# Performance work log

Hardware: AMD Instinct MI355X
Metric: run time of the kernel (lower is better)

## Reference

```python
import jax, jax.numpy as jnp
import numpy as np

N, D = 16384, 32            # nodes, max neighbors (0-padded)
INP, U = 256, 128           # input_units, units
R, ENT = 8, 8               # relations, entity types (relation/entity id 0 = padding for relations)


def setup_inputs() -> dict:
    key = jax.random.key(0)
    ks = jax.random.split(key, 12)
    s = 0.05  # scale learned params for numerical sanity (torch init is raw randn)
    return {
        "node_state": jax.random.normal(ks[0], (N, INP), dtype=jnp.float32),
        "adjacency": jax.random.randint(ks[1], (N, D), 0, N + 1, dtype=jnp.int32),  # 0 = pad row
        "point_enc": jax.random.randint(ks[2], (N,), 0, ENT, dtype=jnp.int32),
        "relation_enc": jax.random.randint(ks[3], (N, D), 0, R, dtype=jnp.int32),   # 0 = pad edge
        "point_enc_w": jax.random.normal(ks[4], (ENT, INP, U), dtype=jnp.float32) * s,
        "relation_enc_w": jax.random.normal(ks[5], (R, U, U), dtype=jnp.float32) * s,
        "q_w": jax.random.normal(ks[6], (U, U), dtype=jnp.float32) * s,
        "k_w": jax.random.normal(ks[7], (U, U), dtype=jnp.float32) * s,
        "v_w": jax.random.normal(ks[8], (U, U), dtype=jnp.float32) * s,
        "fc_w": jax.random.normal(ks[9], (U, U), dtype=jnp.float32) * s,
        "fc_b": jax.random.normal(ks[10], (U,), dtype=jnp.float32) * s,
    }


def reference(node_state, adjacency, point_enc, relation_enc,
              point_enc_w, relation_enc_w, q_w, k_w, v_w, fc_w, fc_b):
    ent, inp, u = point_enc_w.shape
    r_cnt = relation_enc_w.shape[0]
    dt = node_state.dtype

    # center = node_state @ point_enc_w[point_enc]; loop over small fixed entity set
    # to avoid materializing an (N, INP, U) gathered weight tensor.
    center = jnp.zeros((node_state.shape[0], u), dtype=dt)
    for e in range(ent):
        center = center + jnp.where(point_enc[:, None] == e,
                                    node_state @ point_enc_w[e], 0.0)

    # prepend zero row: adjacency index 0 == padding neighbor
    padded = jnp.concatenate([jnp.zeros((1, u), dtype=dt), center], axis=0)  # (N+1, U)
    x = padded[adjacency]  # (N, D, U) gathered neighbor embeddings

    # neighbors = x @ relation_enc_w[relation_enc]; per-relation GEMM + mask
    # (same math as the per-edge gathered matmul, without the E*U*U blowup)
    neighbors = jnp.zeros_like(x)
    for r in range(r_cnt):
        neighbors = neighbors + jnp.where(relation_enc[..., None] == r,
                                          jnp.einsum('ndu,uv->ndv', x, relation_enc_w[r]), 0.0)

    scale = u ** 0.5
    q = (center @ q_w) / scale                               # (N, U)
    k = jnp.einsum('ndu,uv->ndv', neighbors, k_w) / scale    # (N, D, U)
    v = jnp.einsum('ndu,uv->ndv', neighbors, v_w)            # (N, D, U)

    scores = jnp.einsum('nu,ndu->nd', q, k)                  # (N, D)
    scores = jnp.where(relation_enc == 0, jnp.asarray(-1e9, dt), scores)
    attn = jax.nn.softmax(scores, axis=-1)                   # over neighbors
    agg = jnp.einsum('nd,ndu->nu', attn, v)                  # (N, U)

    return center + jax.nn.relu(agg @ fc_w + fc_b)           # (N, U)
```

## Files before the change

kernel.cpp:

```cpp
#include <hip/hip_runtime.h>

#define NNODE 16384
#define DD 32
#define INPC 256
#define UC 128
#define RC 8
#define EC 8

typedef __attribute__((ext_vector_type(8))) short short8;
typedef __attribute__((ext_vector_type(4))) float float4v;
typedef __attribute__((ext_vector_type(4))) unsigned uint4v;

__device__ __forceinline__ unsigned short f2bf(float f) {
    unsigned u = __builtin_bit_cast(unsigned, f);
    unsigned r = (u + 0x7FFFu + ((u >> 16) & 1u)) >> 16;
    return (unsigned short)r;
}
__device__ __forceinline__ float bf2f(unsigned short s) { return __builtin_bit_cast(float, (unsigned)s << 16); }

__device__ __forceinline__ short8 ld8bf(const float* p) {
    float4 v0 = *(const float4*)p;
    float4 v1 = *(const float4*)(p + 4);
    short8 a;
    a[0] = (short)f2bf(v0.x); a[1] = (short)f2bf(v0.y);
    a[2] = (short)f2bf(v0.z); a[3] = (short)f2bf(v0.w);
    a[4] = (short)f2bf(v1.x); a[5] = (short)f2bf(v1.y);
    a[6] = (short)f2bf(v1.z); a[7] = (short)f2bf(v1.w);
    return a;
}

__device__ __forceinline__ int bfrag_idx(int k, int col, int nct) {
    int ks = k >> 5, ct = col >> 4;
    int l = (((k >> 3) & 3) << 4) | (col & 15);
    return (((ks * nct + ct) << 6) + l) * 8 + (k & 7);
}

__global__ void k_setup(const float* __restrict__ pew, const float* __restrict__ qw,
                        const float* __restrict__ kw, const float* __restrict__ relw,
                        const float* __restrict__ vw, const float* __restrict__ fcw,
                        const int* __restrict__ pe,
                        unsigned short* __restrict__ pewfrag,
                        unsigned short* __restrict__ BallQfrag, unsigned short* __restrict__ RVFfrag,
                        int* __restrict__ blockhist) {
    __shared__ unsigned short stage_s[128 * 132];
    __shared__ unsigned short mat_s[16 * 136];
    __shared__ int hh[8];
    int b = blockIdx.x;
    if (b < 1024) {
        int id = b * 256 + threadIdx.x;
        int e = id >> 15, k = (id >> 7) & 255, col = id & 127;
        pewfrag[(e << 15) + bfrag_idx(k, col, 8)] = f2bf(pew[id]);
        return;
    }
    if (b < 1088) {
        int pb = b - 1024;
        int r = pb & 7, i0 = (pb >> 3) * 16;
        int w = threadIdx.x >> 6, l = threadIdx.x & 63;
        int mrow = l & 15, kgrp = (l >> 4) << 3;
        const float* R = relw + r * (UC * UC);

        float4v accP[2] = {};
        #pragma unroll
        for (int ks = 0; ks < 4; ++ks) {
            short8 a = ld8bf(&qw[(i0 + mrow) * UC + ks * 32 + kgrp]);
            #pragma unroll
            for (int ci = 0; ci < 2; ++ci) {
                int ct = w * 2 + ci;
                short8 bf = ld8bf(&kw[(ct * 16 + mrow) * UC + ks * 32 + kgrp]);
                accP[ci] = __builtin_amdgcn_mfma_f32_16x16x32_bf16(a, bf, accP[ci], 0, 0, 0);
            }
        }
        #pragma unroll
        for (int ci = 0; ci < 2; ++ci)
            #pragma unroll
            for (int reg = 0; reg < 4; ++reg) {
                int row = ((l >> 4) << 2) + reg;
                int col = (w * 2 + ci) * 16 + mrow;
                mat_s[row * 136 + col] = f2bf(accP[ci][reg] * (1.0f / 128.0f));
            }
        for (int it = 0; it < 16; ++it) {
            int idx = it * 256 + threadIdx.x;
            int row = idx >> 5, col = (idx & 31) * 4;
            float4 v = *(const float4*)&vw[row * UC + col];
            uint2 o;
            o.x = (unsigned)f2bf(v.x) | ((unsigned)f2bf(v.y) << 16);
            o.y = (unsigned)f2bf(v.z) | ((unsigned)f2bf(v.w) << 16);
            *(uint2*)&stage_s[row * 132 + col] = o;
        }
        __syncthreads();

        float4v accM[2] = {}, accV[2] = {};
        #pragma unroll
        for (int ks = 0; ks < 4; ++ks) {
            short8 aM = *(const short8*)&mat_s[mrow * 136 + ks * 32 + kgrp];
            short8 aV = ld8bf(&R[(i0 + mrow) * UC + ks * 32 + kgrp]);
            #pragma unroll
            for (int ci = 0; ci < 2; ++ci) {
                int ct = w * 2 + ci;
                short8 bM = ld8bf(&R[(ct * 16 + mrow) * UC + ks * 32 + kgrp]);
                accM[ci] = __builtin_amdgcn_mfma_f32_16x16x32_bf16(aM, bM, accM[ci], 0, 0, 0);
                uint4v pv;
                #pragma unroll
                for (int jp = 0; jp < 4; ++jp) {
                    unsigned e0 = stage_s[(ks * 32 + kgrp + jp * 2) * 132 + ct * 16 + mrow];
                    unsigned e1 = stage_s[(ks * 32 + kgrp + jp * 2 + 1) * 132 + ct * 16 + mrow];
                    pv[jp] = e0 | (e1 << 16);
                }
                accV[ci] = __builtin_amdgcn_mfma_f32_16x16x32_bf16(
                    aV, __builtin_bit_cast(short8, pv), accV[ci], 0, 0, 0);
            }
        }
        #pragma unroll
        for (int ci = 0; ci < 2; ++ci)
            #pragma unroll
            for (int reg = 0; reg < 4; ++reg) {
                int i = i0 + ((l >> 4) << 2) + reg;
                int col = r * 128 + (w * 2 + ci) * 16 + mrow;
                BallQfrag[bfrag_idx(i, col, 64)] = f2bf(accM[ci][reg]);
            }
        __syncthreads();
        #pragma unroll
        for (int ci = 0; ci < 2; ++ci)
            #pragma unroll
            for (int reg = 0; reg < 4; ++reg)
                mat_s[(((l >> 4) << 2) + reg) * 136 + (w * 2 + ci) * 16 + mrow] = f2bf(accV[ci][reg]);
        for (int it = 0; it < 16; ++it) {
            int idx = it * 256 + threadIdx.x;
            int row = idx >> 5, col = (idx & 31) * 4;
            float4 v = *(const float4*)&fcw[row * UC + col];
            uint2 o;
            o.x = (unsigned)f2bf(v.x) | ((unsigned)f2bf(v.y) << 16);
            o.y = (unsigned)f2bf(v.z) | ((unsigned)f2bf(v.w) << 16);
            *(uint2*)&stage_s[row * 132 + col] = o;
        }
        __syncthreads();

        float4v accF[2] = {};
        #pragma unroll
        for (int ks = 0; ks < 4; ++ks) {
            short8 aF = *(const short8*)&mat_s[mrow * 136 + ks * 32 + kgrp];
            #pragma unroll
            for (int ci = 0; ci < 2; ++ci) {
                int ct = w * 2 + ci;
                uint4v pv;
                #pragma unroll
                for (int jp = 0; jp < 4; ++jp) {
                    unsigned e0 = stage_s[(ks * 32 + kgrp + jp * 2) * 132 + ct * 16 + mrow];
                    unsigned e1 = stage_s[(ks * 32 + kgrp + jp * 2 + 1) * 132 + ct * 16 + mrow];
                    pv[jp] = e0 | (e1 << 16);
                }
                accF[ci] = __builtin_amdgcn_mfma_f32_16x16x32_bf16(
                    aF, __builtin_bit_cast(short8, pv), accF[ci], 0, 0, 0);
            }
        }
        #pragma unroll
        for (int ci = 0; ci < 2; ++ci)
            #pragma unroll
            for (int reg = 0; reg < 4; ++reg) {
                int i = i0 + ((l >> 4) << 2) + reg;
                int col = (w * 2 + ci) * 16 + mrow;
                RVFfrag[bfrag_idx(r * 128 + i, col, 8)] = f2bf(accF[ci][reg]);
            }
        return;
    }
    {
        int hb = b - 1088;
        if (threadIdx.x < 8) hh[threadIdx.x] = 0;
        __syncthreads();
        atomicAdd(&hh[pe[hb * 256 + threadIdx.x]], 1);
        __syncthreads();
        if (threadIdx.x < 8) blockhist[hb * 8 + threadIdx.x] = hh[threadIdx.x];
    }
}

__global__ void k_scatter(const int* __restrict__ pe, const int* __restrict__ blockhist,
                          int* __restrict__ list, int* __restrict__ cnt, int* __restrict__ basep) {
    __shared__ int boff[8];
    __shared__ int totS[8], exS[8];
    __shared__ int wavecnt[4 * 8];
    int t = threadIdx.x, w = t >> 6, l = t & 63;
    if (w == 0) {
        #pragma unroll
        for (int e = 0; e < 8; ++e) {
            int h = blockhist[l * 8 + e];
            int pref = h;
            #pragma unroll
            for (int off = 1; off < 64; off <<= 1) {
                int v = __shfl_up(pref, off, 64);
                pref += (l >= off) ? v : 0;
            }
            if (l == (int)blockIdx.x) exS[e] = pref - h;
            if (l == 63) totS[e] = pref;
        }
    }
    __syncthreads();
    if (t == 0) {
        int run = 0;
        #pragma unroll
        for (int e = 0; e < 8; ++e) {
            boff[e] = run + exS[e];
            if (blockIdx.x == 0) { basep[e] = run; cnt[e] = totS[e]; }
            run += totS[e];
        }
    }
    __syncthreads();
    int n = blockIdx.x * 256 + t;
    int e = pe[n];
    unsigned long long mymask = 0;
    #pragma unroll
    for (int r = 0; r < 8; ++r) {
        unsigned long long m = __ballot(e == r);
        if (e == r) mymask = m;
        if (l == r) wavecnt[w * 8 + r] = (int)__popcll(m);
    }
    __syncthreads();
    int off = 0;
    for (int w2 = 0; w2 < w; ++w2) off += wavecnt[w2 * 8 + e];
    unsigned long long ltmask = (1ull << l) - 1ull;
    int rank = (int)__popcll(mymask & ltmask);
    list[boff[e] + off + rank] = n;
}

__global__ __launch_bounds__(256, 4)
void k_center(const float* __restrict__ ns, const unsigned short* __restrict__ pewfrag,
              const int* __restrict__ list, const int* __restrict__ cnt,
              const int* __restrict__ base, unsigned short* __restrict__ center_bf) {
    int e = blockIdx.y;
    int c = cnt[e];
    int start = blockIdx.x * 16;
    if (start >= c) return;
    int w = threadIdx.x >> 6, l = threadIdx.x & 63;

    int rid = list[base[e] + min(start + (l & 15), c - 1)];

    float4v acc[2] = {};
    const unsigned short* pf = pewfrag + ((size_t)e << 15);
    #pragma unroll
    for (int ks = 0; ks < 8; ++ks) {
        short8 a = ld8bf(&ns[(size_t)rid * 256 + ks * 32 + ((l >> 4) << 3)]);
        #pragma unroll
        for (int ci = 0; ci < 2; ++ci) {
            int ct = w * 2 + ci;
            short8 b = *(const short8*)&pf[(((ks * 8 + ct) << 6) + l) * 8];
            acc[ci] = __builtin_amdgcn_mfma_f32_16x16x32_bf16(a, b, acc[ci], 0, 0, 0);
        }
    }
    #pragma unroll
    for (int reg = 0; reg < 4; ++reg) {
        int row16 = start + ((l >> 4) << 2) + reg;
        if (row16 < c) {
            int gid = list[base[e] + row16];
            #pragma unroll
            for (int ci = 0; ci < 2; ++ci)
                center_bf[(size_t)gid * 128 + (w * 2 + ci) * 16 + (l & 15)] = f2bf(acc[ci][reg]);
        }
    }
}

#define QSTRIDE 1096
__global__ __launch_bounds__(256, 2)
void k_final(const unsigned short* __restrict__ center_bf,
             const unsigned short* __restrict__ BallQfrag,
             const unsigned short* __restrict__ RVFfrag,
             const int* __restrict__ adj, const int* __restrict__ rel,
             const float* __restrict__ fcb, float* __restrict__ out) {
    __shared__ unsigned short qlds[16 * QSTRIDE];
    __shared__ __align__(16) unsigned short xs[4][4096];
    __shared__ unsigned edata[4][32];
    int w = threadIdx.x >> 6, l = threadIdx.x & 63;
    int n0 = blockIdx.x * 16;

    int aiq[4][2], rvq[4][2], myrow[4];
    #pragma unroll
    for (int q = 0; q < 4; ++q) {
        int n = n0 + w * 4 + q;
        #pragma unroll
        for (int t = 0; t < 2; ++t) {
            aiq[q][t] = adj[n * DD + t * 16 + (l & 15)];
            rvq[q][t] = rel[n * DD + t * 16 + (l & 15)];
        }
    }
    #pragma unroll
    for (int q = 0; q < 4; ++q) {
        int r0 = aiq[q][0] > 0 ? aiq[q][0] - 1 : 0;
        int r1 = aiq[q][1] > 0 ? aiq[q][1] - 1 : 0;
        int s0 = __shfl(r0, (l >> 1) & 15, 64);
        int s1 = __shfl(r1, (l >> 1) & 15, 64);
        myrow[q] = (l >= 32) ? s1 : s0;
    }
    uint4v sb[8];
    #pragma unroll
    for (int i = 0; i < 8; ++i)
        sb[i] = *(const uint4v*)&center_bf[(size_t)myrow[0] * 128 + ((l & 1) + 2 * i) * 8];

    {
        short8 a[4];
        #pragma unroll
        for (int ks = 0; ks < 4; ++ks)
            a[ks] = *(const short8*)&center_bf[(size_t)(n0 + (l & 15)) * 128 + ks * 32 + ((l >> 4) << 3)];
        for (int ci = 0; ci < 16; ++ci) {
            int ct = w * 16 + ci;
            float4v acc = {};
            #pragma unroll
            for (int ks = 0; ks < 4; ++ks) {
                short8 b = *(const short8*)&BallQfrag[(((ks * 64 + ct) << 6) + l) * 8];
                acc = __builtin_amdgcn_mfma_f32_16x16x32_bf16(a[ks], b, acc, 0, 0, 0);
            }
            int r = ct >> 3;
            int ch = (ct & 7) * 16 + (l & 15);
            #pragma unroll
            for (int reg = 0; reg < 4; ++reg) {
                int rn = ((l >> 4) << 2) + reg;
                qlds[rn * QSTRIDE + r * 136 + ch] = f2bf(acc[reg]);
            }
        }
    }
    __syncthreads();

    #pragma unroll
    for (int q = 0; q < 4; ++q) {
        int tn = w * 4 + q;
        int ai[2] = {aiq[q][0], aiq[q][1]};
        int rv[2] = {rvq[q][0], rvq[q][1]};

        #pragma unroll
        for (int i = 0; i < 8; ++i)
            *(uint4v*)&xs[w][i * 512 + (l >> 3) * 64
                             + ((((l >> 1) & 3) ^ ((l >> 3) & 3))) * 16 + (l & 1) * 8] = sb[i];
        if (q < 3) {
            #pragma unroll
            for (int i = 0; i < 8; ++i)
                sb[i] = *(const uint4v*)&center_bf[(size_t)myrow[q + 1] * 128 + ((l & 1) + 2 * i) * 8];
        }

        float4v sc[2] = {};
        #pragma unroll
        for (int ks = 0; ks < 4; ++ks) {
            short8 qb = *(const short8*)&qlds[tn * QSTRIDE + (l & 7) * 136 + ks * 32 + ((l >> 4) << 3)];
            #pragma unroll
            for (int t = 0; t < 2; ++t) {
                short8 xa = *(const short8*)&xs[w][(2 * ks + (l >> 5)) * 512
                                  + (4 * t + ((l >> 2) & 3)) * 64
                                  + (((l & 3) ^ ((l >> 2) & 3))) * 16 + ((l >> 4) & 1) * 8];
                sc[t] = __builtin_amdgcn_mfma_f32_16x16x32_bf16(xa, qb, sc[t], 0, 0, 0);
            }
        }
        float sel[2][4];
        int ai2[2][4];
        #pragma unroll
        for (int t = 0; t < 2; ++t)
            #pragma unroll
            for (int reg = 0; reg < 4; ++reg) {
                int e2l = ((l >> 4) & 3) * 4 + reg;
                int rd2 = __shfl(rv[t], (l & 48) | e2l, 64);
                ai2[t][reg] = __shfl(ai[t], (l & 48) | e2l, 64);
                float s = __shfl(sc[t][reg], (l & 48) | rd2, 64);
                if (ai2[t][reg] == 0) s = 0.f;
                if (rd2 == 0) s = -1e9f;
                sel[t][reg] = s;
            }
        float mx = sel[0][0];
        #pragma unroll
        for (int t = 0; t < 2; ++t)
            #pragma unroll
            for (int reg = 0; reg < 4; ++reg) mx = fmaxf(mx, sel[t][reg]);
        mx = fmaxf(mx, __shfl_xor(mx, 16, 64));
        mx = fmaxf(mx, __shfl_xor(mx, 32, 64));
        float at[2][4];
        float sm = 0.f;
        #pragma unroll
        for (int t = 0; t < 2; ++t)
            #pragma unroll
            for (int reg = 0; reg < 4; ++reg) {
                at[t][reg] = __expf(sel[t][reg] - mx);
                sm += at[t][reg];
            }
        sm += __shfl_xor(sm, 16, 64);
        sm += __shfl_xor(sm, 32, 64);
        float inv = 1.0f / sm;
        #pragma unroll
        for (int t = 0; t < 2; ++t)
            #pragma unroll
            for (int reg = 0; reg < 4; ++reg) {
                at[t][reg] *= inv;
                if (ai2[t][reg] == 0) at[t][reg] = 0.f;
            }

        #pragma unroll
        for (int rg = 0; rg < 4; ++rg) {
            if (l == (l >> 4) * 20 + rg) {
                #pragma unroll
                for (int t = 0; t < 2; ++t)
                    edata[w][t * 16 + (l & 15)] = (unsigned)f2bf(at[t][rg]) | ((unsigned)rv[t] << 16);
            }
        }

        unsigned aw[4];
        #pragma unroll
        for (int jp = 0; jp < 4; ++jp) {
            unsigned m0 = edata[w][((l >> 4) << 3) + jp * 2];
            unsigned m1 = edata[w][((l >> 4) << 3) + jp * 2 + 1];
            unsigned s0 = ((m0 >> 16) == (unsigned)(l & 15)) ? (m0 & 0xFFFFu) : 0u;
            unsigned s1 = ((m1 >> 16) == (unsigned)(l & 15)) ? (m1 & 0xFFFFu) : 0u;
            aw[jp] = s0 | (s1 << 16);
        }
        uint4v av = {aw[0], aw[1], aw[2], aw[3]};
        short8 afrag = __builtin_bit_cast(short8, av);

        #pragma unroll
        for (int ct = 0; ct < 8; ++ct) {
            unsigned short p[8];
            #pragma unroll
            for (int jj = 0; jj < 8; ++jj) {
                int st = (l >> 4) * 2 + (jj >> 2);
                int slot = (jj & 3) ^ (st & 3);
                p[jj] = xs[w][ct * 512 + st * 64 + slot * 16 + (l & 15)];
            }
            uint4v bv = {(unsigned)p[0] | ((unsigned)p[1] << 16),
                         (unsigned)p[2] | ((unsigned)p[3] << 16),
                         (unsigned)p[4] | ((unsigned)p[5] << 16),
                         (unsigned)p[6] | ((unsigned)p[7] << 16)};
            float4v zc = {};
            float4v acc = __builtin_amdgcn_mfma_f32_16x16x32_bf16(
                afrag, __builtin_bit_cast(short8, bv), zc, 0, 0, 0);
            if (l < 32) {
                int rbase = (l >> 4) << 2;
                #pragma unroll
                for (int reg = 0; reg < 4; ++reg)
                    qlds[tn * QSTRIDE + (rbase + reg) * 136 + ct * 16 + (l & 15)] = f2bf(acc[reg]);
            }
        }
    }
    __syncthreads();

    #pragma unroll
    for (int ci = 0; ci < 2; ++ci) {
        int ct = w * 2 + ci;
        float4v acc = {};
        #pragma unroll 4
        for (int ks = 0; ks < 32; ++ks) {
            short8 a = *(const short8*)&qlds[(l & 15) * QSTRIDE + (ks >> 2) * 136
                                             + (ks & 3) * 32 + ((l >> 4) << 3)];
            short8 b = *(const short8*)&RVFfrag[(((ks * 8 + ct) << 6) + l) * 8];
            acc = __builtin_amdgcn_mfma_f32_16x16x32_bf16(a, b, acc, 0, 0, 0);
        }
        int col = ct * 16 + (l & 15);
        float bb = fcb[col];
        #pragma unroll
        for (int reg = 0; reg < 4; ++reg) {
            int n = n0 + ((l >> 4) << 2) + reg;
            float v = acc[reg] + bb;
            v = v > 0.f ? v : 0.f;
            out[(size_t)n * 128 + col] = bf2f(center_bf[(size_t)n * 128 + col]) + v;
        }
    }
}

extern "C" void kernel_launch(void* const* d_in, const int* in_sizes, int n_in,
                              void* d_out, int out_size, void* d_ws, size_t ws_size,
                              hipStream_t stream) {
    const float* node_state = (const float*)d_in[0];
    const int*   adjacency  = (const int*)d_in[1];
    const int*   point_enc  = (const int*)d_in[2];
    const int*   relation   = (const int*)d_in[3];
    const float* pew        = (const float*)d_in[4];
    const float* relw       = (const float*)d_in[5];
    const float* qw         = (const float*)d_in[6];
    const float* kw         = (const float*)d_in[7];
    const float* vw         = (const float*)d_in[8];
    const float* fcw        = (const float*)d_in[9];
    const float* fcb        = (const float*)d_in[10];
    float* out = (float*)d_out;

    char* ws = (char*)d_ws;
    unsigned short* BallQfrag = (unsigned short*)ws;  ws += 128 * 1024 * 2;
    unsigned short* RVFfrag   = (unsigned short*)ws;  ws += 1024 * 128 * 2;
    unsigned short* center_bf = (unsigned short*)ws;  ws += (size_t)NNODE * 128 * 2;
    unsigned short* pewfrag   = (unsigned short*)ws;  ws += 8 * 32768 * 2;
    int* blockhist            = (int*)ws;             ws += 64 * 8 * 4;
    int* cnt                  = (int*)ws;             ws += 32;
    int* basep                = (int*)ws;             ws += 32;
    int* list                 = (int*)ws;             ws += NNODE * 4;

    k_setup<<<1152, 256, 0, stream>>>(pew, qw, kw, relw, vw, fcw, point_enc,
                                      pewfrag, BallQfrag, RVFfrag, blockhist);
    k_scatter<<<64, 256, 0, stream>>>(point_enc, blockhist, list, cnt, basep);
    k_center<<<dim3(192, 8), 256, 0, stream>>>(node_state, pewfrag, list, cnt, basep, center_bf);
    k_final<<<NNODE / 16, 256, 0, stream>>>(center_bf, BallQfrag, RVFfrag,
                                            adjacency, relation, fcb, out);
}
```

Before: 160.2 us.

## Load score MFMA operands directly from global and pair-pack neighbor rows in LDS

The score MFMA now reads neighbor embedding fragments straight from global memory into registers, and prefetches the next node's fragments, instead of reading them back from an LDS staging tile. The LDS tile used for the attention-weighted aggregation is rebuilt with a new layout that interleaves pairs of neighbor rows into 32-bit words. The B-fragment for that MFMA then needs four 32-bit LDS reads instead of eight 16-bit reads plus packing. The trade-off is more global loads per node and more register pressure from the prefetched fragments.

```diff
diff --git a/kernel.cpp b/kernel.cpp
--- a/kernel.cpp
+++ b/kernel.cpp
@@ -270,7 +270,7 @@
     int w = threadIdx.x >> 6, l = threadIdx.x & 63;
     int n0 = blockIdx.x * 16;
 
-    int aiq[4][2], rvq[4][2], myrow[4];
+    int aiq[4][2], rvq[4][2], rvrow[4][2];
     #pragma unroll
     for (int q = 0; q < 4; ++q) {
         int n = n0 + w * 4 + q;
@@ -278,20 +278,16 @@
         for (int t = 0; t < 2; ++t) {
             aiq[q][t] = adj[n * DD + t * 16 + (l & 15)];
             rvq[q][t] = rel[n * DD + t * 16 + (l & 15)];
-        }
-    }
-    #pragma unroll
-    for (int q = 0; q < 4; ++q) {
-        int r0 = aiq[q][0] > 0 ? aiq[q][0] - 1 : 0;
-        int r1 = aiq[q][1] > 0 ? aiq[q][1] - 1 : 0;
-        int s0 = __shfl(r0, (l >> 1) & 15, 64);
-        int s1 = __shfl(r1, (l >> 1) & 15, 64);
-        myrow[q] = (l >= 32) ? s1 : s0;
-    }
-    uint4v sb[8];
-    #pragma unroll
-    for (int i = 0; i < 8; ++i)
-        sb[i] = *(const uint4v*)&center_bf[(size_t)myrow[0] * 128 + ((l & 1) + 2 * i) * 8];
+            rvrow[q][t] = aiq[q][t] > 0 ? aiq[q][t] - 1 : 0;
+        }
+    }
+
+    short8 xp[2][4];
+    #pragma unroll
+    for (int t = 0; t < 2; ++t)
+        #pragma unroll
+        for (int ks = 0; ks < 4; ++ks)
+            xp[t][ks] = *(const short8*)&center_bf[(size_t)rvrow[0][t] * 128 + ks * 32 + ((l >> 4) << 3)];
 
     {
         short8 a[4];
@@ -317,20 +313,25 @@
     }
     __syncthreads();
 
+    unsigned* xsw = (unsigned*)&xs[w][0];
+
     #pragma unroll
     for (int q = 0; q < 4; ++q) {
         int tn = w * 4 + q;
         int ai[2] = {aiq[q][0], aiq[q][1]};
         int rv[2] = {rvq[q][0], rvq[q][1]};
 
-        #pragma unroll
-        for (int i = 0; i < 8; ++i)
-            *(uint4v*)&xs[w][i * 512 + (l >> 3) * 64
-                             + ((((l >> 1) & 3) ^ ((l >> 3) & 3))) * 16 + (l & 1) * 8] = sb[i];
-        if (q < 3) {
-            #pragma unroll
-            for (int i = 0; i < 8; ++i)
-                sb[i] = *(const uint4v*)&center_bf[(size_t)myrow[q + 1] * 128 + ((l & 1) + 2 * i) * 8];
+        int srcA = (l >> 1) & 14, srcB = srcA | 1;
+        int a0 = __shfl(rvrow[q][0], srcA, 64), a1 = __shfl(rvrow[q][1], srcA, 64);
+        int b0 = __shfl(rvrow[q][0], srcB, 64), b1 = __shfl(rvrow[q][1], srcB, 64);
+        int rA = (l >= 32) ? a1 : a0;
+        int rB = (l >= 32) ? b1 : b0;
+        uint4v sbA[4], sbB[4];
+        #pragma unroll
+        for (int i = 0; i < 4; ++i) {
+            int c = (l & 3) + 4 * i;
+            sbA[i] = *(const uint4v*)&center_bf[(size_t)rA * 128 + c * 8];
+            sbB[i] = *(const uint4v*)&center_bf[(size_t)rB * 128 + c * 8];
         }
 
         float4v sc[2] = {};
@@ -338,13 +339,18 @@
         for (int ks = 0; ks < 4; ++ks) {
             short8 qb = *(const short8*)&qlds[tn * QSTRIDE + (l & 7) * 136 + ks * 32 + ((l >> 4) << 3)];
             #pragma unroll
-            for (int t = 0; t < 2; ++t) {
-                short8 xa = *(const short8*)&xs[w][(2 * ks + (l >> 5)) * 512
-                                  + (4 * t + ((l >> 2) & 3)) * 64
-                                  + (((l & 3) ^ ((l >> 2) & 3))) * 16 + ((l >> 4) & 1) * 8];
-                sc[t] = __builtin_amdgcn_mfma_f32_16x16x32_bf16(xa, qb, sc[t], 0, 0, 0);
-            }
-        }
+            for (int t = 0; t < 2; ++t)
+                sc[t] = __builtin_amdgcn_mfma_f32_16x16x32_bf16(xp[t][ks], qb, sc[t], 0, 0, 0);
+        }
+        if (q < 3) {
+            #pragma unroll
+            for (int t = 0; t < 2; ++t)
+                #pragma unroll
+                for (int ks = 0; ks < 4; ++ks)
+                    xp[t][ks] = *(const short8*)&center_bf[(size_t)rvrow[q + 1][t] * 128
+                                                           + ks * 32 + ((l >> 4) << 3)];
+        }
+
         float sel[2][4];
         int ai2[2][4];
         #pragma unroll
@@ -407,19 +413,36 @@
         uint4v av = {aw[0], aw[1], aw[2], aw[3]};
         short8 afrag = __builtin_bit_cast(short8, av);
 
+        {
+            unsigned p = (unsigned)(l >> 2);
+            unsigned xorb = ((l >> 4) & 1u) << 4;
+            #pragma unroll
+            for (int i = 0; i < 4; ++i) {
+                int c = (l & 3) + 4 * i;
+                unsigned o[8];
+                #pragma unroll
+                for (int k = 0; k < 4; ++k) {
+                    unsigned A = sbA[i][k], B = sbB[i][k];
+                    o[2 * k]     = (A & 0xFFFFu) | (B << 16);
+                    o[2 * k + 1] = (A >> 16) | (B & 0xFFFF0000u);
+                }
+                unsigned d = p * 128u + (((unsigned)(c * 8)) ^ xorb);
+                uint4v lo = {o[0], o[1], o[2], o[3]};
+                uint4v hi = {o[4], o[5], o[6], o[7]};
+                *(uint4v*)(xsw + d) = lo;
+                *(uint4v*)(xsw + d + 4) = hi;
+            }
+        }
+
         #pragma unroll
         for (int ct = 0; ct < 8; ++ct) {
-            unsigned short p[8];
-            #pragma unroll
-            for (int jj = 0; jj < 8; ++jj) {
-                int st = (l >> 4) * 2 + (jj >> 2);
-                int slot = (jj & 3) ^ (st & 3);
-                p[jj] = xs[w][ct * 512 + st * 64 + slot * 16 + (l & 15)];
-            }
-            uint4v bv = {(unsigned)p[0] | ((unsigned)p[1] << 16),
-                         (unsigned)p[2] | ((unsigned)p[3] << 16),
-                         (unsigned)p[4] | ((unsigned)p[5] << 16),
-                         (unsigned)p[6] | ((unsigned)p[7] << 16)};
+            uint4v bv;
+            #pragma unroll
+            for (int m = 0; m < 4; ++m) {
+                unsigned p2 = (unsigned)((l >> 4) * 4 + m);
+                unsigned ch = (unsigned)(ct * 16 + (l & 15));
+                bv[m] = xsw[p2 * 128u + (ch ^ (((l >> 4) & 1u) << 4))];
+            }
             float4v zc = {};
             float4v acc = __builtin_amdgcn_mfma_f32_16x16x32_bf16(
                 afrag, __builtin_bit_cast(short8, bv), zc, 0, 0, 0);
```

New measurement: 166.1 us. 3.7% more time.

## Load neighbor rows directly as MFMA fragments and keep softmax in registers

Applied to the files above, without the earlier changes.

Neighbor center rows are now loaded straight into MFMA operand layout (xp) and used from registers for the score MFMA, swapping operand order so each lane holds one edge's scores. The LDS copy uses a new row-major swizzle and is read only by the aggregation step. Softmax is done with lane-per-edge shuffles instead of an 8-way gather, and the edata LDS exchange is replaced by shuffles. The final FC loop is restructured to share A loads across two output tiles. In exchange it uses more registers (32 VGPRs for xp) and does strided 16-bit LDS reads that may hit bank conflicts.

```diff
diff --git a/kernel.cpp b/kernel.cpp
--- a/kernel.cpp
+++ b/kernel.cpp
@@ -266,11 +266,10 @@
              const float* __restrict__ fcb, float* __restrict__ out) {
     __shared__ unsigned short qlds[16 * QSTRIDE];
     __shared__ __align__(16) unsigned short xs[4][4096];
-    __shared__ unsigned edata[4][32];
     int w = threadIdx.x >> 6, l = threadIdx.x & 63;
     int n0 = blockIdx.x * 16;
 
-    int aiq[4][2], rvq[4][2], myrow[4];
+    int aiq[4][2], rvq[4][2], rvrow[4][2];
     #pragma unroll
     for (int q = 0; q < 4; ++q) {
         int n = n0 + w * 4 + q;
@@ -278,20 +277,16 @@
         for (int t = 0; t < 2; ++t) {
             aiq[q][t] = adj[n * DD + t * 16 + (l & 15)];
             rvq[q][t] = rel[n * DD + t * 16 + (l & 15)];
-        }
-    }
-    #pragma unroll
-    for (int q = 0; q < 4; ++q) {
-        int r0 = aiq[q][0] > 0 ? aiq[q][0] - 1 : 0;
-        int r1 = aiq[q][1] > 0 ? aiq[q][1] - 1 : 0;
-        int s0 = __shfl(r0, (l >> 1) & 15, 64);
-        int s1 = __shfl(r1, (l >> 1) & 15, 64);
-        myrow[q] = (l >= 32) ? s1 : s0;
-    }
-    uint4v sb[8];
-    #pragma unroll
-    for (int i = 0; i < 8; ++i)
-        sb[i] = *(const uint4v*)&center_bf[(size_t)myrow[0] * 128 + ((l & 1) + 2 * i) * 8];
+            rvrow[q][t] = aiq[q][t] > 0 ? aiq[q][t] - 1 : 0;
+        }
+    }
+
+    short8 xp[2][4];
+    #pragma unroll
+    for (int t = 0; t < 2; ++t)
+        #pragma unroll
+        for (int ks = 0; ks < 4; ++ks)
+            xp[t][ks] = *(const short8*)&center_bf[(size_t)rvrow[0][t] * 128 + ks * 32 + ((l >> 4) << 3)];
 
     {
         short8 a[4];
@@ -317,89 +312,89 @@
     }
     __syncthreads();
 
+    unsigned short* xsw = &xs[w][0];
+
     #pragma unroll
     for (int q = 0; q < 4; ++q) {
         int tn = w * 4 + q;
-        int ai[2] = {aiq[q][0], aiq[q][1]};
-        int rv[2] = {rvq[q][0], rvq[q][1]};
-
-        #pragma unroll
-        for (int i = 0; i < 8; ++i)
-            *(uint4v*)&xs[w][i * 512 + (l >> 3) * 64
-                             + ((((l >> 1) & 3) ^ ((l >> 3) & 3))) * 16 + (l & 1) * 8] = sb[i];
-        if (q < 3) {
-            #pragma unroll
-            for (int i = 0; i < 8; ++i)
-                sb[i] = *(const uint4v*)&center_bf[(size_t)myrow[q + 1] * 128 + ((l & 1) + 2 * i) * 8];
+        int ai0 = aiq[q][0], ai1 = aiq[q][1];
+        int rv0 = rvq[q][0], rv1 = rvq[q][1];
+
+        #pragma unroll
+        for (int t = 0; t < 2; ++t) {
+            int edge = t * 16 + (l & 15);
+            unsigned swz = (((unsigned)edge >> 3) & 3u) << 4;
+            #pragma unroll
+            for (int ks = 0; ks < 4; ++ks) {
+                unsigned ch0 = (unsigned)(ks * 32 + ((l >> 4) << 3));
+                *(short8*)&xsw[(unsigned)(edge * 128) + (ch0 ^ swz)] = xp[t][ks];
+            }
         }
 
         float4v sc[2] = {};
         #pragma unroll
         for (int ks = 0; ks < 4; ++ks) {
             short8 qb = *(const short8*)&qlds[tn * QSTRIDE + (l & 7) * 136 + ks * 32 + ((l >> 4) << 3)];
-            #pragma unroll
-            for (int t = 0; t < 2; ++t) {
-                short8 xa = *(const short8*)&xs[w][(2 * ks + (l >> 5)) * 512
-                                  + (4 * t + ((l >> 2) & 3)) * 64
-                                  + (((l & 3) ^ ((l >> 2) & 3))) * 16 + ((l >> 4) & 1) * 8];
-                sc[t] = __builtin_amdgcn_mfma_f32_16x16x32_bf16(xa, qb, sc[t], 0, 0, 0);
-            }
-        }
-        float sel[2][4];
-        int ai2[2][4];
-        #pragma unroll
-        for (int t = 0; t < 2; ++t)
-            #pragma unroll
-            for (int reg = 0; reg < 4; ++reg) {
-                int e2l = ((l >> 4) & 3) * 4 + reg;
-                int rd2 = __shfl(rv[t], (l & 48) | e2l, 64);
-                ai2[t][reg] = __shfl(ai[t], (l & 48) | e2l, 64);
-                float s = __shfl(sc[t][reg], (l & 48) | rd2, 64);
-                if (ai2[t][reg] == 0) s = 0.f;
-                if (rd2 == 0) s = -1e9f;
-                sel[t][reg] = s;
-            }
-        float mx = sel[0][0];
-        #pragma unroll
-        for (int t = 0; t < 2; ++t)
-            #pragma unroll
-            for (int reg = 0; reg < 4; ++reg) mx = fmaxf(mx, sel[t][reg]);
-        mx = fmaxf(mx, __shfl_xor(mx, 16, 64));
-        mx = fmaxf(mx, __shfl_xor(mx, 32, 64));
-        float at[2][4];
-        float sm = 0.f;
-        #pragma unroll
-        for (int t = 0; t < 2; ++t)
-            #pragma unroll
-            for (int reg = 0; reg < 4; ++reg) {
-                at[t][reg] = __expf(sel[t][reg] - mx);
-                sm += at[t][reg];
-            }
-        sm += __shfl_xor(sm, 16, 64);
-        sm += __shfl_xor(sm, 32, 64);
+            sc[0] = __builtin_amdgcn_mfma_f32_16x16x32_bf16(qb, xp[0][ks], sc[0], 0, 0, 0);
+            sc[1] = __builtin_amdgcn_mfma_f32_16x16x32_bf16(qb, xp[1][ks], sc[1], 0, 0, 0);
+        }
+
+        if (q < 3) {
+            #pragma unroll
+            for (int t = 0; t < 2; ++t)
+                #pragma unroll
+                for (int ks = 0; ks < 4; ++ks)
+                    xp[t][ks] = *(const short8*)&center_bf[(size_t)rvrow[q + 1][t] * 128
+                                                           + ks * 32 + ((l >> 4) << 3)];
+        }
+
+        float sel0, sel1;
+        {
+            int r = rv0;
+            float v01 = (r & 1) ? sc[0][1] : sc[0][0];
+            float v23 = (r & 1) ? sc[0][3] : sc[0][2];
+            float regv = (r & 2) ? v23 : v01;
+            float s = __shfl(regv, ((r >> 2) << 4) | (l & 15), 64);
+            if (ai0 == 0) s = 0.f;
+            if (r == 0) s = -1e9f;
+            sel0 = s;
+        }
+        {
+            int r = rv1;
+            float v01 = (r & 1) ? sc[1][1] : sc[1][0];
+            float v23 = (r & 1) ? sc[1][3] : sc[1][2];
+            float regv = (r & 2) ? v23 : v01;
+            float s = __shfl(regv, ((r >> 2) << 4) | (l & 15), 64);
+            if (ai1 == 0) s = 0.f;
+            if (r == 0) s = -1e9f;
+            sel1 = s;
+        }
+
+        float mx = fmaxf(sel0, sel1);
+        mx = fmaxf(mx, __shfl_xor(mx, 1, 64));
+        mx = fmaxf(mx, __shfl_xor(mx, 2, 64));
+        mx = fmaxf(mx, __shfl_xor(mx, 4, 64));
+        mx = fmaxf(mx, __shfl_xor(mx, 8, 64));
+        float at0 = __expf(sel0 - mx);
+        float at1 = __expf(sel1 - mx);
+        float sm = at0 + at1;
+        sm += __shfl_xor(sm, 1, 64);
+        sm += __shfl_xor(sm, 2, 64);
+        sm += __shfl_xor(sm, 4, 64);
+        sm += __shfl_xor(sm, 8, 64);
         float inv = 1.0f / sm;
-        #pragma unroll
-        for (int t = 0; t < 2; ++t)
-            #pragma unroll
-            for (int reg = 0; reg < 4; ++reg) {
-                at[t][reg] *= inv;
-                if (ai2[t][reg] == 0) at[t][reg] = 0.f;
-            }
-
-        #pragma unroll
-        for (int rg = 0; rg < 4; ++rg) {
-            if (l == (l >> 4) * 20 + rg) {
-                #pragma unroll
-                for (int t = 0; t < 2; ++t)
-                    edata[w][t * 16 + (l & 15)] = (unsigned)f2bf(at[t][rg]) | ((unsigned)rv[t] << 16);
-            }
-        }
-
+        at0 *= inv; at1 *= inv;
+        if (ai0 == 0) at0 = 0.f;
+        if (ai1 == 0) at1 = 0.f;
+
+        unsigned md0 = (unsigned)f2bf(at0) | ((unsigned)rv0 << 16);
+        unsigned md1 = (unsigned)f2bf(at1) | ((unsigned)rv1 << 16);
+        unsigned mdsel = (l >= 32) ? md1 : md0;
         unsigned aw[4];
         #pragma unroll
         for (int jp = 0; jp < 4; ++jp) {
-            unsigned m0 = edata[w][((l >> 4) << 3) + jp * 2];
-            unsigned m1 = edata[w][((l >> 4) << 3) + jp * 2 + 1];
+            unsigned m0 = __shfl(mdsel, (l & 48) | (((l >> 4) & 1) * 8 + jp * 2), 64);
+            unsigned m1 = __shfl(mdsel, (l & 48) | (((l >> 4) & 1) * 8 + jp * 2 + 1), 64);
             unsigned s0 = ((m0 >> 16) == (unsigned)(l & 15)) ? (m0 & 0xFFFFu) : 0u;
             unsigned s1 = ((m1 >> 16) == (unsigned)(l & 15)) ? (m1 & 0xFFFFu) : 0u;
             aw[jp] = s0 | (s1 << 16);
@@ -412,9 +407,10 @@
             unsigned short p[8];
             #pragma unroll
             for (int jj = 0; jj < 8; ++jj) {
-                int st = (l >> 4) * 2 + (jj >> 2);
-                int slot = (jj & 3) ^ (st & 3);
-                p[jj] = xs[w][ct * 512 + st * 64 + slot * 16 + (l & 15)];
+                int edge = (l >> 4) * 8 + jj;
+                unsigned addr = (unsigned)(edge * 128)
+                              + (((unsigned)(ct * 16 + (l & 15))) ^ ((((unsigned)edge >> 3) & 3u) << 4));
+                p[jj] = xsw[addr];
             }
             uint4v bv = {(unsigned)p[0] | ((unsigned)p[1] << 16),
                          (unsigned)p[2] | ((unsigned)p[3] << 16),
@@ -433,25 +429,31 @@
     }
     __syncthreads();
 
-    #pragma unroll
-    for (int ci = 0; ci < 2; ++ci) {
-        int ct = w * 2 + ci;
-        float4v acc = {};
+    {
+        float4v acc[2] = {};
         #pragma unroll 4
         for (int ks = 0; ks < 32; ++ks) {
             short8 a = *(const short8*)&qlds[(l & 15) * QSTRIDE + (ks >> 2) * 136
                                              + (ks & 3) * 32 + ((l >> 4) << 3)];
-            short8 b = *(const short8*)&RVFfrag[(((ks * 8 + ct) << 6) + l) * 8];
-            acc = __builtin_amdgcn_mfma_f32_16x16x32_bf16(a, b, acc, 0, 0, 0);
-        }
-        int col = ct * 16 + (l & 15);
-        float bb = fcb[col];
-        #pragma unroll
-        for (int reg = 0; reg < 4; ++reg) {
-            int n = n0 + ((l >> 4) << 2) + reg;
-            float v = acc[reg] + bb;
-            v = v > 0.f ? v : 0.f;
-            out[(size_t)n * 128 + col] = bf2f(center_bf[(size_t)n * 128 + col]) + v;
+            #pragma unroll
+            for (int ci = 0; ci < 2; ++ci) {
+                int ct = w * 2 + ci;
+                short8 b = *(const short8*)&RVFfrag[(((ks * 8 + ct) << 6) + l) * 8];
+                acc[ci] = __builtin_amdgcn_mfma_f32_16x16x32_bf16(a, b, acc[ci], 0, 0, 0);
+            }
+        }
+        #pragma unroll
+        for (int ci = 0; ci < 2; ++ci) {
+            int ct = w * 2 + ci;
+            int col = ct * 16 + (l & 15);
+            float bb = fcb[col];
+            #pragma unroll
+            for (int reg = 0; reg < 4; ++reg) {
+                int n = n0 + ((l >> 4) << 2) + reg;
+                float v = acc[ci][reg] + bb;
+                v = v > 0.f ? v : 0.f;
+                out[(size_t)n * 128 + col] = bf2f(center_bf[(size_t)n * 128 + col]) + v;
+            }
         }
     }
 }
```

Result: slower. 169.4 us (+5.7%).
